# Kernel tuning notes

Hardware: AMD Instinct MI355X
Metric: run time of the kernel (lower is better)

## Reference

```python
import jax, jax.numpy as jnp
import numpy as np

B, D, K, E = 256, 256, 1024, 16  # batch, dim_codes, book_size, embedding_dim
DECAY = 0.999
GAIN = 1.0 - DECAY
EPS = 1e-6


def setup_inputs() -> dict:
    key = jax.random.key(0)
    k1, k2 = jax.random.split(key)
    return {
        "cw_q": jax.random.normal(k1, (B, D * E), dtype=jnp.float32),
        "codebook": jax.random.normal(k2, (D, K, E), dtype=jnp.float32),
        "ema_counts": jnp.ones((D, K), dtype=jnp.float32),
    }


def reference(cw_q, codebook, ema_counts):
    batch = cw_q.shape[0]
    x = cw_q.reshape(batch, D, E)  # [B, D, E]

    x2 = jnp.sum(x * x, axis=-1)                       # [B, D]
    c2 = jnp.sum(codebook * codebook, axis=-1)         # [D, K]
    xc = jnp.einsum('bde,dke->bdk', x, codebook)       # [B, D, K]
    dist = x2[:, :, None] + c2[None, :, :] - 2.0 * xc

    idx = jnp.argmin(dist, axis=-1)                    # [B, D] int32

    # gather nearest code vector per (batch, dim_code)
    cw_embed = codebook[jnp.arange(D)[None, :], idx]   # [B, D, E]
    cw_embed = cw_embed.reshape(batch, D * E)

    one_hot_idx = jax.nn.one_hot(idx, K, dtype=cw_q.dtype)  # [B, D, K]

    # EMA update (training path): scatter-sum of assigned vectors per code
    update = jnp.einsum('bdk,bde->dke', one_hot_idx, x)      # [D, K, E]
    new_codebook = codebook * DECAY + GAIN * update / (ema_counts[:, :, None] + EPS)
    new_ema_counts = DECAY * ema_counts + GAIN * jnp.sum(one_hot_idx, axis=0)

    return cw_embed, one_hot_idx, new_codebook, new_ema_counts
```

## Files before the change

kernel.cpp:

```cpp
#include <hip/hip_runtime.h>
#include <float.h>

#define BB 256
#define DD 256
#define KK 1024
#define EE 16
#define DECAY 0.999f
#define GAIN  0.001f
#define EPS   1e-6f

#define OH_OFF   ((size_t)BB * DD * EE)
#define CB_OFF   (OH_OFF + (size_t)BB * DD * KK)
#define EMA_OFF  (CB_OFF + (size_t)DD * KK * EE)

__device__ __forceinline__ float dot16(const float4& a0, const float4& a1,
                                       const float4& a2, const float4& a3,
                                       const float4& b0, const float4& b1,
                                       const float4& b2, const float4& b3) {
  float s = a0.x * b0.x;
  s = fmaf(a0.y, b0.y, s); s = fmaf(a0.z, b0.z, s); s = fmaf(a0.w, b0.w, s);
  s = fmaf(a1.x, b1.x, s); s = fmaf(a1.y, b1.y, s); s = fmaf(a1.z, b1.z, s); s = fmaf(a1.w, b1.w, s);
  s = fmaf(a2.x, b2.x, s); s = fmaf(a2.y, b2.y, s); s = fmaf(a2.z, b2.z, s); s = fmaf(a2.w, b2.w, s);
  s = fmaf(a3.x, b3.x, s); s = fmaf(a3.y, b3.y, s); s = fmaf(a3.z, b3.z, s); s = fmaf(a3.w, b3.w, s);
  return s;
}

__global__ __launch_bounds__(512, 2) void vqvae_fused(
    const float* __restrict__ cw_q,
    const float* __restrict__ codebook,
    const float* __restrict__ ema,
    float* __restrict__ out)
{
  __shared__ float4 cb4s[KK * EE / 4];
  __shared__ float4 upd4s[KK * EE / 4];
  __shared__ float  c2s[KK];
  __shared__ float  cnts[KK];
  __shared__ float  pbest[8 * 256];
  __shared__ int    pidxs[8 * 256];
  __shared__ int    ish[BB];

  const int t = threadIdx.x;
  const int d = blockIdx.x;
  const int w = t >> 6;
  const int l = t & 63;
  const float4 z4 = make_float4(0.f, 0.f, 0.f, 0.f);

  #pragma unroll
  for (int j = 0; j < 2; ++j) cnts[t + 512 * j] = 0.f;
  #pragma unroll
  for (int i = 0; i < 8; ++i) upd4s[i * 512 + t] = z4;

  const float4* src4 = (const float4*)codebook + (size_t)d * (KK * EE / 4);
  #pragma unroll
  for (int i = 0; i < 8; ++i) {
    int i4 = i * 512 + t;
    float4 v = src4[i4];
    cb4s[i4] = v;
    float sq = v.x * v.x;
    sq = fmaf(v.y, v.y, sq);
    sq = fmaf(v.z, v.z, sq);
    sq = fmaf(v.w, v.w, sq);
    sq += __shfl_xor(sq, 1);
    sq += __shfl_xor(sq, 2);
    if ((t & 3) == 0) c2s[i4 >> 2] = sq;
  }

  float4 xv[4][4];
  float  x2[4];
  #pragma unroll
  for (int j = 0; j < 4; ++j) {
    const int b = l + 64 * j;
    const float4* xr = (const float4*)cw_q + (size_t)b * (DD * EE / 4) + d * 4;
    xv[j][0] = xr[0]; xv[j][1] = xr[1]; xv[j][2] = xr[2]; xv[j][3] = xr[3];
  }
  __syncthreads();

  #pragma unroll
  for (int j = 0; j < 4; ++j)
    x2[j] = dot16(xv[j][0], xv[j][1], xv[j][2], xv[j][3],
                  xv[j][0], xv[j][1], xv[j][2], xv[j][3]);

  float best[4] = {FLT_MAX, FLT_MAX, FLT_MAX, FLT_MAX};
  int   bi[4]   = {0, 0, 0, 0};
  const int kbase = w << 7;

  float* ohp = out + OH_OFF;
  float4* zb = (float4*)(ohp + (size_t)(w << 5) * (DD * KK) + (size_t)d * KK) + l;

  #pragma unroll 2
  for (int s = 0; s < 128; ++s) {
    const int k = kbase + s;
    const float4* p = cb4s + (k << 2);
    float4 c0 = p[0], c1 = p[1], c2v = p[2], c3 = p[3];
    const float c2k = c2s[k];

    #pragma unroll
    for (int j = 0; j < 4; ++j) {
      float dj = dot16(c0, c1, c2v, c3, xv[j][0], xv[j][1], xv[j][2], xv[j][3]);
      float dist = fmaf(-2.f, dj, x2[j] + c2k);
      if (dist < best[j]) { best[j] = dist; bi[j] = k; }
    }

    zb[(size_t)(s >> 2) * (DD * KK / 4) + (s & 3) * 64] = z4;
  }

  #pragma unroll
  for (int j = 0; j < 4; ++j) {
    pbest[w * 256 + l + 64 * j] = best[j];
    pidxs[w * 256 + l + 64 * j] = bi[j];
  }
  __syncthreads();

  if (t < 256) {
    const int b = t;
    float bb = pbest[b];
    int   bidx = pidxs[b];
    #pragma unroll
    for (int w2 = 1; w2 < 8; ++w2) {
      float e = pbest[w2 * 256 + b];
      int   ii = pidxs[w2 * 256 + b];
      if (e < bb) { bb = e; bidx = ii; }
    }

    float4* ce = (float4*)out + (size_t)b * (DD * EE / 4) + d * 4;
    const float4* cwp = cb4s + (bidx << 2);
    ce[0] = cwp[0]; ce[1] = cwp[1]; ce[2] = cwp[2]; ce[3] = cwp[3];

    ohp[(size_t)b * (DD * KK) + (size_t)d * KK + bidx] = 1.0f;

    ish[b] = bidx;
    atomicAdd(&cnts[bidx], 1.0f);
  }
  __syncthreads();

  {
    float* upd = (float*)upd4s;
    const int e = t & 15;
    const int g = t >> 4;
    #pragma unroll
    for (int i = 0; i < 8; ++i) {
      int b = g * 8 + i;
      int k = ish[b];
      float xvv = cw_q[(size_t)b * (DD * EE) + (size_t)d * EE + e];
      atomicAdd(&upd[k * EE + e], xvv);
    }
  }
  __syncthreads();

  {
    const float* emad = ema + (size_t)d * KK;
    float* oe = out + EMA_OFF + (size_t)d * KK;
    #pragma unroll
    for (int j = 0; j < 2; ++j) {
      int k = t + 512 * j;
      float ev = emad[k];
      c2s[k] = ev;
      oe[k] = DECAY * ev + GAIN * cnts[k];
    }
  }
  __syncthreads();

  {
    float4* ocb = (float4*)(out + CB_OFF) + (size_t)d * (KK * EE / 4);
    #pragma unroll
    for (int i = 0; i < 8; ++i) {
      int i4 = i * 512 + t;
      int k  = i4 >> 2;
      float4 c = cb4s[i4];
      float4 u = upd4s[i4];
      float inv = GAIN / (c2s[k] + EPS);
      float4 r;
      r.x = DECAY * c.x + u.x * inv;
      r.y = DECAY * c.y + u.y * inv;
      r.z = DECAY * c.z + u.z * inv;
      r.w = DECAY * c.w + u.w * inv;
      ocb[i4] = r;
    }
  }
}

extern "C" void kernel_launch(void* const* d_in, const int* in_sizes, int n_in,
                              void* d_out, int out_size, void* d_ws, size_t ws_size,
                              hipStream_t stream) {
  const float* cw_q     = (const float*)d_in[0];
  const float* codebook = (const float*)d_in[1];
  const float* ema      = (const float*)d_in[2];
  float* out = (float*)d_out;
  (void)in_sizes; (void)n_in; (void)out_size; (void)d_ws; (void)ws_size;

  vqvae_fused<<<dim3(DD), dim3(512), 0, stream>>>(cw_q, codebook, ema, out);
}
```

Baseline: 326.1 us.

## Split one-hot output writing into a separate coalesced fill kernel

Moves the 256 MB one-hot zero-fill and the scattered 1.0 writes out of the distance/argmin kernel. The first kernel now stores argmin indices to workspace, and a second grid-stride kernel writes the whole one-hot tensor as contiguous float4 values computed from those indices. This aims to stop the strided zero stores from competing with the compute loop and to give the large store fully coalesced, high-occupancy streaming. The cost is an extra launch and a serial dependency, so the dominant write is no longer overlapped with the distance compute.

```diff
diff --git a/kernel.cpp b/kernel.cpp
--- a/kernel.cpp
+++ b/kernel.cpp
@@ -25,11 +25,12 @@
   return s;
 }
 
-__global__ __launch_bounds__(512, 2) void vqvae_fused(
+__global__ __launch_bounds__(512, 2) void vq_assign_update(
     const float* __restrict__ cw_q,
     const float* __restrict__ codebook,
     const float* __restrict__ ema,
-    float* __restrict__ out)
+    float* __restrict__ out,
+    int* __restrict__ idx_ws)
 {
   __shared__ float4 cb4s[KK * EE / 4];
   __shared__ float4 upd4s[KK * EE / 4];
@@ -84,9 +85,6 @@
   int   bi[4]   = {0, 0, 0, 0};
   const int kbase = w << 7;
 
-  float* ohp = out + OH_OFF;
-  float4* zb = (float4*)(ohp + (size_t)(w << 5) * (DD * KK) + (size_t)d * KK) + l;
-
   #pragma unroll 2
   for (int s = 0; s < 128; ++s) {
     const int k = kbase + s;
@@ -100,8 +98,6 @@
       float dist = fmaf(-2.f, dj, x2[j] + c2k);
       if (dist < best[j]) { best[j] = dist; bi[j] = k; }
     }
-
-    zb[(size_t)(s >> 2) * (DD * KK / 4) + (s & 3) * 64] = z4;
   }
 
   #pragma unroll
@@ -126,8 +122,7 @@
     const float4* cwp = cb4s + (bidx << 2);
     ce[0] = cwp[0]; ce[1] = cwp[1]; ce[2] = cwp[2]; ce[3] = cwp[3];
 
-    ohp[(size_t)b * (DD * KK) + (size_t)d * KK + bidx] = 1.0f;
-
+    idx_ws[(size_t)b * DD + d] = bidx;
     ish[b] = bidx;
     atomicAdd(&cnts[bidx], 1.0f);
   }
@@ -179,14 +174,37 @@
   }
 }
 
+__global__ __launch_bounds__(256) void vq_onehot_fill(
+    const int* __restrict__ idx_ws,
+    float* __restrict__ out)
+{
+  const size_t total4 = (size_t)BB * DD * KK / 4;
+  float4* oh4 = (float4*)(out + OH_OFF);
+  const size_t stride = (size_t)gridDim.x * blockDim.x;
+  for (size_t q = (size_t)blockIdx.x * blockDim.x + threadIdx.x;
+       q < total4; q += stride) {
+    const int r = (int)(q >> 8);
+    const int c = ((int)q & 255) << 2;
+    const int idx = idx_ws[r];
+    float4 v;
+    v.x = (idx == c)     ? 1.0f : 0.0f;
+    v.y = (idx == c + 1) ? 1.0f : 0.0f;
+    v.z = (idx == c + 2) ? 1.0f : 0.0f;
+    v.w = (idx == c + 3) ? 1.0f : 0.0f;
+    oh4[q] = v;
+  }
+}
+
 extern "C" void kernel_launch(void* const* d_in, const int* in_sizes, int n_in,
                               void* d_out, int out_size, void* d_ws, size_t ws_size,
                               hipStream_t stream) {
   const float* cw_q     = (const float*)d_in[0];
   const float* codebook = (const float*)d_in[1];
   const float* ema      = (const float*)d_in[2];
-  float* out = (float*)d_out;
-  (void)in_sizes; (void)n_in; (void)out_size; (void)d_ws; (void)ws_size;
-
-  vqvae_fused<<<dim3(DD), dim3(512), 0, stream>>>(cw_q, codebook, ema, out);
-}
+  float* out  = (float*)d_out;
+  int* idx_ws = (int*)d_ws;
+  (void)in_sizes; (void)n_in; (void)out_size; (void)ws_size;
+
+  vq_assign_update<<<dim3(DD), dim3(512), 0, stream>>>(cw_q, codebook, ema, out, idx_ws);
+  vq_onehot_fill<<<dim3(4096), dim3(256), 0, stream>>>(idx_ws, out);
+}
```

Result: slower. 341.1 us (+4.6%).
